# Performance work log

Measured on AMD Instinct MI355X. Metric: run time of the kernel, lower is better.

Reference implementation:

```python
import jax, jax.numpy as jnp
import numpy as np

EPS = 1e-12  # matches torch.nn.functional.normalize eps


def _normalize(x):
    n = jnp.sqrt(jnp.sum(x * x, axis=-1, keepdims=True))
    return x / jnp.maximum(n, EPS)


def setup_inputs() -> dict:
    key = jax.random.key(0)
    k1, k2, k3 = jax.random.split(key, 3)
    B, C, D = 1024, 32768, 512
    embeddings = jax.random.normal(k1, (B, D), dtype=jnp.float32)
    proxies = jax.random.normal(k2, (C, D), dtype=jnp.float32) / 8.0
    labels = jax.random.randint(k3, (B,), 0, C, dtype=jnp.int64)
    return {"embeddings": embeddings, "proxies": proxies, "labels": labels}


def reference(embeddings, proxies, labels):
    # batch: [B, D], P: [C, D], both scaled to norm 3
    batch = 3.0 * _normalize(embeddings)
    P = 3.0 * _normalize(proxies)

    # Squared euclidean distances to ALL proxies via the expansion
    # ||b - p||^2 = ||b||^2 + ||p||^2 - 2 b.p  -> [B, C]
    b_sq = jnp.sum(batch * batch, axis=-1, keepdims=True)      # [B, 1]
    p_sq = jnp.sum(P * P, axis=-1)                             # [C]
    dist = b_sq + p_sq[None, :] - 2.0 * (batch @ P.T)          # [B, C]

    B = batch.shape[0]
    rows = jnp.arange(B)
    pos_dist = dist[rows, labels]                              # [B]

    # logsumexp over negatives: mask out the positive class per row
    neg_scores = jnp.where(
        jnp.arange(dist.shape[1])[None, :] == labels[:, None],
        -jnp.inf,
        -dist,
    )
    neg_lse = jax.nn.logsumexp(neg_scores, axis=1)             # [B]

    return jnp.mean(pos_dist + neg_lse)
```

## Files before the change

kernel.cpp:

```cpp
#include <hip/hip_runtime.h>
#include <stdint.h>

#define D_DIM 512
#define B_ROWS 1024
#define C_ROWS 32768
#define NBLK (C_ROWS / 128)

typedef __attribute__((ext_vector_type(8))) short short8;
typedef __attribute__((ext_vector_type(4))) float floatx4;

#define GLOBAL_AS __attribute__((address_space(1)))
#define LDS_AS __attribute__((address_space(3)))

__device__ inline unsigned short f2bf(float f) {
    unsigned u = __float_as_uint(f);
    u += 0x7fffu + ((u >> 16) & 1u);
    return (unsigned short)(u >> 16);
}

__device__ inline void async_copy16(const unsigned short* g, unsigned short* l) {
    __builtin_amdgcn_global_load_lds((const GLOBAL_AS void*)g, (LDS_AS void*)l, 16, 0, 0);
}

__global__ void norm_rows_kernel(const float* __restrict__ prox,
                                 const float* __restrict__ emb,
                                 unsigned short* __restrict__ Pbf,
                                 unsigned short* __restrict__ Abf) {
    const int wid = threadIdx.x >> 6;
    const int lane = threadIdx.x & 63;
    int row = blockIdx.x * 4 + wid;
    const float* src;
    unsigned short* dst;
    if (row < C_ROWS) {
        src = prox; dst = Pbf;
    } else {
        row -= C_ROWS;
        src = emb; dst = Abf;
    }

    const float4* p = (const float4*)(src + (size_t)row * D_DIM + lane * 8);
    float4 v0 = p[0];
    float4 v1 = p[1];
    float ss = v0.x * v0.x + v0.y * v0.y + v0.z * v0.z + v0.w * v0.w +
               v1.x * v1.x + v1.y * v1.y + v1.z * v1.z + v1.w * v1.w;
#pragma unroll
    for (int off = 1; off < 64; off <<= 1) ss += __shfl_xor(ss, off);
    const float s = 3.0f * rsqrtf(ss);

    unsigned short h[8];
    h[0] = f2bf(v0.x * s); h[1] = f2bf(v0.y * s);
    h[2] = f2bf(v0.z * s); h[3] = f2bf(v0.w * s);
    h[4] = f2bf(v1.x * s); h[5] = f2bf(v1.y * s);
    h[6] = f2bf(v1.z * s); h[7] = f2bf(v1.w * s);
    uint4 packed;
    packed.x = (unsigned)h[0] | ((unsigned)h[1] << 16);
    packed.y = (unsigned)h[2] | ((unsigned)h[3] << 16);
    packed.z = (unsigned)h[4] | ((unsigned)h[5] << 16);
    packed.w = (unsigned)h[6] | ((unsigned)h[7] << 16);
    *(uint4*)(dst + (size_t)row * D_DIM + lane * 8) = packed;
}

__global__ void __launch_bounds__(256)
gemm_lse_kernel(const unsigned short* __restrict__ A,
                const unsigned short* __restrict__ Bm,
                float* __restrict__ part) {
    __shared__ unsigned short sA[2][128 * 32];
    __shared__ unsigned short sB[2][128 * 32];
    __shared__ float red[128];

    const int tid = threadIdx.x;
    const int wid = tid >> 6;
    const int lane = tid & 63;
    const int m0 = blockIdx.x * 128;
    const int n0 = blockIdx.y * 128;

    if (tid < 128) red[tid] = 0.f;

    const int srow = wid * 16 + (lane >> 2);
    const int sg = lane & 3;
    const int gl = (sg - ((lane >> 3) & 3)) & 3;
    const unsigned short* gA = A + (size_t)(m0 + srow) * D_DIM + gl * 8;
    const unsigned short* gB = Bm + (size_t)(n0 + srow) * D_DIM + gl * 8;
    const int loff = srow * 32 + sg * 8;

    const int wm = (wid >> 1) * 64;
    const int wn = (wid & 1) * 64;
    const int fr = lane & 15;
    const int quad = lane >> 4;
    const int swz = (((quad + ((fr >> 1) & 3)) & 3) * 8);

    floatx4 acc[4][4];
    const floatx4 zero = {0.f, 0.f, 0.f, 0.f};
#pragma unroll
    for (int i = 0; i < 4; ++i)
#pragma unroll
        for (int j = 0; j < 4; ++j) acc[i][j] = zero;

    for (int kk = 0; kk < D_DIM; kk += 64) {
        async_copy16(gA + kk,                   &sA[0][loff]);
        async_copy16(gA + kk + 64 * D_DIM,      &sA[0][loff + 64 * 32]);
        async_copy16(gA + kk + 32,              &sA[1][loff]);
        async_copy16(gA + kk + 32 + 64 * D_DIM, &sA[1][loff + 64 * 32]);
        async_copy16(gB + kk,                   &sB[0][loff]);
        async_copy16(gB + kk + 64 * D_DIM,      &sB[0][loff + 64 * 32]);
        async_copy16(gB + kk + 32,              &sB[1][loff]);
        async_copy16(gB + kk + 32 + 64 * D_DIM, &sB[1][loff + 64 * 32]);
        __syncthreads();

#pragma unroll
        for (int c = 0; c < 2; ++c) {
            short8 af[4], bfv[4];
#pragma unroll
            for (int t = 0; t < 4; ++t) {
                af[t]  = *(const short8*)&sA[c][(wm + t * 16 + fr) * 32 + swz];
                bfv[t] = *(const short8*)&sB[c][(wn + t * 16 + fr) * 32 + swz];
            }
#pragma unroll
            for (int ti = 0; ti < 4; ++ti)
#pragma unroll
                for (int tj = 0; tj < 4; ++tj)
                    acc[ti][tj] = __builtin_amdgcn_mfma_f32_16x16x32_bf16(
                        af[ti], bfv[tj], acc[ti][tj], 0, 0, 0);
        }
        __syncthreads();
    }

#pragma unroll
    for (int ti = 0; ti < 4; ++ti) {
        float rs[4] = {0.f, 0.f, 0.f, 0.f};
#pragma unroll
        for (int tj = 0; tj < 4; ++tj)
#pragma unroll
            for (int r = 0; r < 4; ++r)
                rs[r] += __expf(2.0f * acc[ti][tj][r]);
#pragma unroll
        for (int r = 0; r < 4; ++r) {
            rs[r] += __shfl_xor(rs[r], 1);
            rs[r] += __shfl_xor(rs[r], 2);
            rs[r] += __shfl_xor(rs[r], 4);
            rs[r] += __shfl_xor(rs[r], 8);
        }
        if (fr == 0) {
#pragma unroll
            for (int r = 0; r < 4; ++r)
                atomicAdd(&red[wm + ti * 16 + quad * 4 + r], rs[r]);
        }
    }
    __syncthreads();
    if (tid < 128) part[(size_t)(m0 + tid) * NBLK + blockIdx.y] = red[tid];
}

__global__ void rowloss_kernel(const float* __restrict__ part,
                               const unsigned short* __restrict__ A,
                               const unsigned short* __restrict__ Bm,
                               const int* __restrict__ labels,
                               float* __restrict__ rowloss) {
    const int wid = threadIdx.x >> 6;
    const int lane = threadIdx.x & 63;
    const int b = blockIdx.x * 4 + wid;
    if (b >= B_ROWS) return;

    float4 pv = *(const float4*)&part[(size_t)b * NBLK + lane * 4];
    float s = pv.x + pv.y + pv.z + pv.w;

    const int l = labels[b];
    uint4 ua = *(const uint4*)(A + (size_t)b * D_DIM + lane * 8);
    uint4 ub = *(const uint4*)(Bm + (size_t)l * D_DIM + lane * 8);
    const unsigned* au = (const unsigned*)&ua;
    const unsigned* bu = (const unsigned*)&ub;
    float d = 0.f;
#pragma unroll
    for (int j = 0; j < 4; ++j) {
        float a0 = __uint_as_float(au[j] << 16);
        float a1 = __uint_as_float(au[j] & 0xffff0000u);
        float b0 = __uint_as_float(bu[j] << 16);
        float b1 = __uint_as_float(bu[j] & 0xffff0000u);
        d += a0 * b0 + a1 * b1;
    }
#pragma unroll
    for (int off = 1; off < 64; off <<= 1) {
        s += __shfl_xor(s, off);
        d += __shfl_xor(d, off);
    }
    if (lane == 0) {
        float p2 = 2.0f * d;
        rowloss[b] = logf(s - __expf(p2)) - p2;
    }
}

__global__ void finalize_kernel(const float* __restrict__ rowloss,
                                float* __restrict__ out) {
    __shared__ float red[4];
    const int tid = threadIdx.x;
    float local = 0.f;
    for (int b = tid; b < B_ROWS; b += 256) local += rowloss[b];
#pragma unroll
    for (int off = 1; off < 64; off <<= 1) local += __shfl_xor(local, off);
    const int wid = tid >> 6;
    const int lane = tid & 63;
    if (lane == 0) red[wid] = local;
    __syncthreads();
    if (tid == 0) out[0] = (red[0] + red[1] + red[2] + red[3]) / (float)B_ROWS;
}

extern "C" void kernel_launch(void* const* d_in, const int* in_sizes, int n_in,
                              void* d_out, int out_size, void* d_ws, size_t ws_size,
                              hipStream_t stream) {
    const float* emb = (const float*)d_in[0];
    const float* prox = (const float*)d_in[1];
    const int* labels = (const int*)d_in[2];
    float* out = (float*)d_out;

    char* ws = (char*)d_ws;
    unsigned short* Pbf = (unsigned short*)ws;
    unsigned short* Abf = (unsigned short*)(ws + (size_t)C_ROWS * D_DIM * 2);
    float* part = (float*)(ws + (size_t)C_ROWS * D_DIM * 2 + (size_t)B_ROWS * D_DIM * 2);
    float* rowloss = part + (size_t)B_ROWS * NBLK;

    norm_rows_kernel<<<(C_ROWS + B_ROWS) / 4, 256, 0, stream>>>(prox, emb, Pbf, Abf);
    gemm_lse_kernel<<<dim3(B_ROWS / 128, NBLK), 256, 0, stream>>>(Abf, Pbf, part);
    rowloss_kernel<<<B_ROWS / 4, 256, 0, stream>>>(part, Abf, Pbf, labels, rowloss);
    finalize_kernel<<<1, 256, 0, stream>>>(rowloss, out);
}
```

Baseline: 153.4 us.

## Pre-swizzle bf16 operands into MFMA fragment layout and load directly to registers

The normalization kernel now writes A and P in a tiled layout that matches the per-lane MFMA fragment order, so the GEMM kernel can read fragments straight from global memory into registers with double buffering and no LDS staging or barriers. Each block now covers 128x512 of the output in two passes over 256 columns, which cuts the grid from 256 to 64 column splits and shrinks the partial-sum buffer. The cost is that every wave loads its own A and B fragments from global/L2 instead of sharing them through LDS, which means more redundant memory traffic, and register pressure is higher under the (256,2) launch bounds.

```diff
diff --git a/kernel.cpp b/kernel.cpp
--- a/kernel.cpp
+++ b/kernel.cpp
@@ -4,13 +4,11 @@
 #define D_DIM 512
 #define B_ROWS 1024
 #define C_ROWS 32768
-#define NBLK (C_ROWS / 128)
+#define NSPLIT 64
+#define NCHUNK 16
 
 typedef __attribute__((ext_vector_type(8))) short short8;
 typedef __attribute__((ext_vector_type(4))) float floatx4;
-
-#define GLOBAL_AS __attribute__((address_space(1)))
-#define LDS_AS __attribute__((address_space(3)))
 
 __device__ inline unsigned short f2bf(float f) {
     unsigned u = __float_as_uint(f);
@@ -18,14 +16,11 @@
     return (unsigned short)(u >> 16);
 }
 
-__device__ inline void async_copy16(const unsigned short* g, unsigned short* l) {
-    __builtin_amdgcn_global_load_lds((const GLOBAL_AS void*)g, (LDS_AS void*)l, 16, 0, 0);
-}
-
-__global__ void norm_rows_kernel(const float* __restrict__ prox,
-                                 const float* __restrict__ emb,
-                                 unsigned short* __restrict__ Pbf,
-                                 unsigned short* __restrict__ Abf) {
+
+__global__ void norm_swz_kernel(const float* __restrict__ prox,
+                                const float* __restrict__ emb,
+                                unsigned short* __restrict__ Pbf,
+                                unsigned short* __restrict__ Abf) {
     const int wid = threadIdx.x >> 6;
     const int lane = threadIdx.x & 63;
     int row = blockIdx.x * 4 + wid;
@@ -57,97 +52,122 @@
     packed.y = (unsigned)h[2] | ((unsigned)h[3] << 16);
     packed.z = (unsigned)h[4] | ((unsigned)h[5] << 16);
     packed.w = (unsigned)h[6] | ((unsigned)h[7] << 16);
-    *(uint4*)(dst + (size_t)row * D_DIM + lane * 8) = packed;
-}
-
-__global__ void __launch_bounds__(256)
-gemm_lse_kernel(const unsigned short* __restrict__ A,
-                const unsigned short* __restrict__ Bm,
+
+    const size_t unit = ((size_t)(row >> 4) * 16 + (lane >> 2)) * 64 +
+                        (lane & 3) * 16 + (row & 15);
+    *(uint4*)(dst + unit * 8) = packed;
+}
+
+__global__ void __launch_bounds__(256, 2)
+gemm_lse_kernel(const unsigned short* __restrict__ Ap,
+                const unsigned short* __restrict__ Bp,
                 float* __restrict__ part) {
-    __shared__ unsigned short sA[2][128 * 32];
-    __shared__ unsigned short sB[2][128 * 32];
     __shared__ float red[128];
 
     const int tid = threadIdx.x;
     const int wid = tid >> 6;
     const int lane = tid & 63;
-    const int m0 = blockIdx.x * 128;
-    const int n0 = blockIdx.y * 128;
+    const int m0t = blockIdx.x * 8;
+    const int n0t = blockIdx.y * 32;
 
     if (tid < 128) red[tid] = 0.f;
 
-    const int srow = wid * 16 + (lane >> 2);
-    const int sg = lane & 3;
-    const int gl = (sg - ((lane >> 3) & 3)) & 3;
-    const unsigned short* gA = A + (size_t)(m0 + srow) * D_DIM + gl * 8;
-    const unsigned short* gB = Bm + (size_t)(n0 + srow) * D_DIM + gl * 8;
-    const int loff = srow * 32 + sg * 8;
-
-    const int wm = (wid >> 1) * 64;
-    const int wn = (wid & 1) * 64;
+    const int wmt = (wid >> 1) * 4;
+    const int wnt = (wid & 1) * 4;
     const int fr = lane & 15;
     const int quad = lane >> 4;
-    const int swz = (((quad + ((fr >> 1) & 3)) & 3) * 8);
-
-    floatx4 acc[4][4];
-    const floatx4 zero = {0.f, 0.f, 0.f, 0.f};
+
+    const unsigned short* Abase = Ap + (size_t)(m0t + wmt) * 8192 + lane * 8;
+
+    float rsacc[4][4];
 #pragma unroll
     for (int i = 0; i < 4; ++i)
 #pragma unroll
-        for (int j = 0; j < 4; ++j) acc[i][j] = zero;
-
-    for (int kk = 0; kk < D_DIM; kk += 64) {
-        async_copy16(gA + kk,                   &sA[0][loff]);
-        async_copy16(gA + kk + 64 * D_DIM,      &sA[0][loff + 64 * 32]);
-        async_copy16(gA + kk + 32,              &sA[1][loff]);
-        async_copy16(gA + kk + 32 + 64 * D_DIM, &sA[1][loff + 64 * 32]);
-        async_copy16(gB + kk,                   &sB[0][loff]);
-        async_copy16(gB + kk + 64 * D_DIM,      &sB[0][loff + 64 * 32]);
-        async_copy16(gB + kk + 32,              &sB[1][loff]);
-        async_copy16(gB + kk + 32 + 64 * D_DIM, &sB[1][loff + 64 * 32]);
-        __syncthreads();
-
-#pragma unroll
-        for (int c = 0; c < 2; ++c) {
-            short8 af[4], bfv[4];
-#pragma unroll
-            for (int t = 0; t < 4; ++t) {
-                af[t]  = *(const short8*)&sA[c][(wm + t * 16 + fr) * 32 + swz];
-                bfv[t] = *(const short8*)&sB[c][(wn + t * 16 + fr) * 32 + swz];
+        for (int r = 0; r < 4; ++r) rsacc[i][r] = 0.f;
+
+#pragma unroll
+    for (int pass = 0; pass < 2; ++pass) {
+        const unsigned short* Bbase =
+            Bp + (size_t)(n0t + pass * 16 + wnt) * 8192 + lane * 8;
+
+        floatx4 acc[2][4][4];
+        const floatx4 zero = {0.f, 0.f, 0.f, 0.f};
+#pragma unroll
+        for (int tt = 0; tt < 2; ++tt)
+#pragma unroll
+            for (int i = 0; i < 4; ++i)
+#pragma unroll
+                for (int j = 0; j < 4; ++j) acc[tt][i][j] = zero;
+
+        short8 abuf[2][4], bbuf[2][2][4];
+#pragma unroll
+        for (int t = 0; t < 4; ++t)
+            abuf[0][t] = *(const short8*)(Abase + t * 8192);
+#pragma unroll
+        for (int tt = 0; tt < 2; ++tt)
+#pragma unroll
+            for (int tj = 0; tj < 4; ++tj)
+                bbuf[0][tt][tj] = *(const short8*)(Bbase + (tt * 8 + tj) * 8192);
+
+#pragma unroll
+        for (int c = 0; c < NCHUNK; ++c) {
+            const int cur = c & 1, nxt = cur ^ 1;
+            if (c < NCHUNK - 1) {
+#pragma unroll
+                for (int t = 0; t < 4; ++t)
+                    abuf[nxt][t] = *(const short8*)(Abase + t * 8192 + (c + 1) * 512);
+#pragma unroll
+                for (int tt = 0; tt < 2; ++tt)
+#pragma unroll
+                    for (int tj = 0; tj < 4; ++tj)
+                        bbuf[nxt][tt][tj] =
+                            *(const short8*)(Bbase + (tt * 8 + tj) * 8192 + (c + 1) * 512);
             }
 #pragma unroll
             for (int ti = 0; ti < 4; ++ti)
 #pragma unroll
+                for (int tt = 0; tt < 2; ++tt)
+#pragma unroll
+                    for (int tj = 0; tj < 4; ++tj)
+                        acc[tt][ti][tj] = __builtin_amdgcn_mfma_f32_16x16x32_bf16(
+                            abuf[cur][ti], bbuf[cur][tt][tj], acc[tt][ti][tj], 0, 0, 0);
+        }
+
+#pragma unroll
+        for (int ti = 0; ti < 4; ++ti)
+#pragma unroll
+            for (int tt = 0; tt < 2; ++tt)
+#pragma unroll
                 for (int tj = 0; tj < 4; ++tj)
-                    acc[ti][tj] = __builtin_amdgcn_mfma_f32_16x16x32_bf16(
-                        af[ti], bfv[tj], acc[ti][tj], 0, 0, 0);
+#pragma unroll
+                    for (int r = 0; r < 4; ++r)
+                        rsacc[ti][r] += __expf(2.0f * acc[tt][ti][tj][r]);
+    }
+
+#pragma unroll
+    for (int ti = 0; ti < 4; ++ti) {
+#pragma unroll
+        for (int r = 0; r < 4; ++r) {
+            float v = rsacc[ti][r];
+            v += __shfl_xor(v, 1);
+            v += __shfl_xor(v, 2);
+            v += __shfl_xor(v, 4);
+            v += __shfl_xor(v, 8);
+            rsacc[ti][r] = v;
         }
-        __syncthreads();
-    }
-
-#pragma unroll
-    for (int ti = 0; ti < 4; ++ti) {
-        float rs[4] = {0.f, 0.f, 0.f, 0.f};
-#pragma unroll
-        for (int tj = 0; tj < 4; ++tj)
+    }
+    __syncthreads();
+    if (fr == 0) {
+        const int wrow = (wid >> 1) * 64;
+#pragma unroll
+        for (int ti = 0; ti < 4; ++ti)
 #pragma unroll
             for (int r = 0; r < 4; ++r)
-                rs[r] += __expf(2.0f * acc[ti][tj][r]);
-#pragma unroll
-        for (int r = 0; r < 4; ++r) {
-            rs[r] += __shfl_xor(rs[r], 1);
-            rs[r] += __shfl_xor(rs[r], 2);
-            rs[r] += __shfl_xor(rs[r], 4);
-            rs[r] += __shfl_xor(rs[r], 8);
-        }
-        if (fr == 0) {
-#pragma unroll
-            for (int r = 0; r < 4; ++r)
-                atomicAdd(&red[wm + ti * 16 + quad * 4 + r], rs[r]);
-        }
+                atomicAdd(&red[wrow + ti * 16 + quad * 4 + r], rsacc[ti][r]);
     }
     __syncthreads();
-    if (tid < 128) part[(size_t)(m0 + tid) * NBLK + blockIdx.y] = red[tid];
+    if (tid < 128)
+        part[(size_t)(blockIdx.x * 128 + tid) * NSPLIT + blockIdx.y] = red[tid];
 }
 
 __global__ void rowloss_kernel(const float* __restrict__ part,
@@ -160,12 +180,15 @@
     const int b = blockIdx.x * 4 + wid;
     if (b >= B_ROWS) return;
 
-    float4 pv = *(const float4*)&part[(size_t)b * NBLK + lane * 4];
-    float s = pv.x + pv.y + pv.z + pv.w;
+    float s = part[(size_t)b * NSPLIT + lane];
 
     const int l = labels[b];
-    uint4 ua = *(const uint4*)(A + (size_t)b * D_DIM + lane * 8);
-    uint4 ub = *(const uint4*)(Bm + (size_t)l * D_DIM + lane * 8);
+    const size_t ub_unit = ((size_t)(b >> 4) * 16 + (lane >> 2)) * 64 +
+                           (lane & 3) * 16 + (b & 15);
+    const size_t ul_unit = ((size_t)(l >> 4) * 16 + (lane >> 2)) * 64 +
+                           (lane & 3) * 16 + (l & 15);
+    uint4 ua = *(const uint4*)(A + ub_unit * 8);
+    uint4 ub = *(const uint4*)(Bm + ul_unit * 8);
     const unsigned* au = (const unsigned*)&ua;
     const unsigned* bu = (const unsigned*)&ub;
     float d = 0.f;
@@ -214,11 +237,11 @@
     char* ws = (char*)d_ws;
     unsigned short* Pbf = (unsigned short*)ws;
     unsigned short* Abf = (unsigned short*)(ws + (size_t)C_ROWS * D_DIM * 2);
-    float* part = (float*)(ws + (size_t)C_ROWS * D_DIM * 2 + (size_t)B_ROWS * D_DIM * 2);
-    float* rowloss = part + (size_t)B_ROWS * NBLK;
-
-    norm_rows_kernel<<<(C_ROWS + B_ROWS) / 4, 256, 0, stream>>>(prox, emb, Pbf, Abf);
-    gemm_lse_kernel<<<dim3(B_ROWS / 128, NBLK), 256, 0, stream>>>(Abf, Pbf, part);
+    float* part = (float*)(ws + (size_t)(C_ROWS + B_ROWS) * D_DIM * 2);
+    float* rowloss = part + (size_t)B_ROWS * NSPLIT;
+
+    norm_swz_kernel<<<(C_ROWS + B_ROWS) / 4, 256, 0, stream>>>(prox, emb, Pbf, Abf);
+    gemm_lse_kernel<<<dim3(B_ROWS / 128, NSPLIT), 256, 0, stream>>>(Abf, Pbf, part);
     rowloss_kernel<<<B_ROWS / 4, 256, 0, stream>>>(part, Abf, Pbf, labels, rowloss);
     finalize_kernel<<<1, 256, 0, stream>>>(rowloss, out);
 }
```

Result: slower. 478.0 us (+211.7%).

## Double-buffer LDS tiles in GEMM-LSE kernel and swap grid dimension order

Applied to the files above, without the earlier changes.

Splits the LDS staging into two buffers so the async global-to-LDS load for the next K chunk is issued before the MFMA work on the current chunk, leaving one barrier per iteration instead of two. It also swaps the grid so blockIdx.x walks proxy (N) tiles and blockIdx.y walks batch tiles, which changes the order in which blocks touch A and B in cache. It adds a launch-bounds hint of two blocks per CU. LDS use doubles to about 64KB per block, which may cap how many blocks fit on a CU.

```diff
diff --git a/kernel.cpp b/kernel.cpp
--- a/kernel.cpp
+++ b/kernel.cpp
@@ -60,19 +60,19 @@
     *(uint4*)(dst + (size_t)row * D_DIM + lane * 8) = packed;
 }
 
-__global__ void __launch_bounds__(256)
+__global__ void __launch_bounds__(256, 2)
 gemm_lse_kernel(const unsigned short* __restrict__ A,
                 const unsigned short* __restrict__ Bm,
                 float* __restrict__ part) {
-    __shared__ unsigned short sA[2][128 * 32];
-    __shared__ unsigned short sB[2][128 * 32];
+    __shared__ unsigned short sA[2][2][128 * 32];
+    __shared__ unsigned short sB[2][2][128 * 32];
     __shared__ float red[128];
 
     const int tid = threadIdx.x;
     const int wid = tid >> 6;
     const int lane = tid & 63;
-    const int m0 = blockIdx.x * 128;
-    const int n0 = blockIdx.y * 128;
+    const int n0 = blockIdx.x * 128;
+    const int m0 = blockIdx.y * 128;
 
     if (tid < 128) red[tid] = 0.f;
 
@@ -87,7 +87,19 @@
     const int wn = (wid & 1) * 64;
     const int fr = lane & 15;
     const int quad = lane >> 4;
-    const int swz = (((quad + ((fr >> 1) & 3)) & 3) * 8);
+    const int swz = ((quad + ((fr >> 1) & 3)) & 3) * 8;
+
+#define STAGE(d, kk)                                                      \
+    do {                                                                  \
+        async_copy16(gA + (kk),                   &sA[d][0][loff]);       \
+        async_copy16(gA + (kk) + 64 * D_DIM,      &sA[d][0][loff + 64 * 32]); \
+        async_copy16(gA + (kk) + 32,              &sA[d][1][loff]);       \
+        async_copy16(gA + (kk) + 32 + 64 * D_DIM, &sA[d][1][loff + 64 * 32]); \
+        async_copy16(gB + (kk),                   &sB[d][0][loff]);       \
+        async_copy16(gB + (kk) + 64 * D_DIM,      &sB[d][0][loff + 64 * 32]); \
+        async_copy16(gB + (kk) + 32,              &sB[d][1][loff]);       \
+        async_copy16(gB + (kk) + 32 + 64 * D_DIM, &sB[d][1][loff + 64 * 32]); \
+    } while (0)
 
     floatx4 acc[4][4];
     const floatx4 zero = {0.f, 0.f, 0.f, 0.f};
@@ -96,24 +108,20 @@
 #pragma unroll
         for (int j = 0; j < 4; ++j) acc[i][j] = zero;
 
-    for (int kk = 0; kk < D_DIM; kk += 64) {
-        async_copy16(gA + kk,                   &sA[0][loff]);
-        async_copy16(gA + kk + 64 * D_DIM,      &sA[0][loff + 64 * 32]);
-        async_copy16(gA + kk + 32,              &sA[1][loff]);
-        async_copy16(gA + kk + 32 + 64 * D_DIM, &sA[1][loff + 64 * 32]);
-        async_copy16(gB + kk,                   &sB[0][loff]);
-        async_copy16(gB + kk + 64 * D_DIM,      &sB[0][loff + 64 * 32]);
-        async_copy16(gB + kk + 32,              &sB[1][loff]);
-        async_copy16(gB + kk + 32 + 64 * D_DIM, &sB[1][loff + 64 * 32]);
+    STAGE(0, 0);
+
+    for (int c = 0; c < 8; ++c) {
+        const int cur = c & 1;
         __syncthreads();
-
-#pragma unroll
-        for (int c = 0; c < 2; ++c) {
+        if (c < 7) STAGE(cur ^ 1, (c + 1) * 64);
+
+#pragma unroll
+        for (int sub = 0; sub < 2; ++sub) {
             short8 af[4], bfv[4];
 #pragma unroll
             for (int t = 0; t < 4; ++t) {
-                af[t]  = *(const short8*)&sA[c][(wm + t * 16 + fr) * 32 + swz];
-                bfv[t] = *(const short8*)&sB[c][(wn + t * 16 + fr) * 32 + swz];
+                af[t]  = *(const short8*)&sA[cur][sub][(wm + t * 16 + fr) * 32 + swz];
+                bfv[t] = *(const short8*)&sB[cur][sub][(wn + t * 16 + fr) * 32 + swz];
             }
 #pragma unroll
             for (int ti = 0; ti < 4; ++ti)
@@ -122,8 +130,8 @@
                     acc[ti][tj] = __builtin_amdgcn_mfma_f32_16x16x32_bf16(
                         af[ti], bfv[tj], acc[ti][tj], 0, 0, 0);
         }
-        __syncthreads();
-    }
+    }
+#undef STAGE
 
 #pragma unroll
     for (int ti = 0; ti < 4; ++ti) {
@@ -147,7 +155,7 @@
         }
     }
     __syncthreads();
-    if (tid < 128) part[(size_t)(m0 + tid) * NBLK + blockIdx.y] = red[tid];
+    if (tid < 128) part[(size_t)(m0 + tid) * NBLK + blockIdx.x] = red[tid];
 }
 
 __global__ void rowloss_kernel(const float* __restrict__ part,
@@ -214,11 +222,11 @@
     char* ws = (char*)d_ws;
     unsigned short* Pbf = (unsigned short*)ws;
     unsigned short* Abf = (unsigned short*)(ws + (size_t)C_ROWS * D_DIM * 2);
-    float* part = (float*)(ws + (size_t)C_ROWS * D_DIM * 2 + (size_t)B_ROWS * D_DIM * 2);
+    float* part = (float*)(ws + (size_t)(C_ROWS + B_ROWS) * D_DIM * 2);
     float* rowloss = part + (size_t)B_ROWS * NBLK;
 
     norm_rows_kernel<<<(C_ROWS + B_ROWS) / 4, 256, 0, stream>>>(prox, emb, Pbf, Abf);
-    gemm_lse_kernel<<<dim3(B_ROWS / 128, NBLK), 256, 0, stream>>>(Abf, Pbf, part);
+    gemm_lse_kernel<<<dim3(NBLK, B_ROWS / 128), 256, 0, stream>>>(Abf, Pbf, part);
     rowloss_kernel<<<B_ROWS / 4, 256, 0, stream>>>(part, Abf, Pbf, labels, rowloss);
     finalize_kernel<<<1, 256, 0, stream>>>(rowloss, out);
 }
```

Measured after the change: 150.0 us. 2.2% less time.
